# Kernel optimization log

Measured on AMD Instinct MI355X. Metric: run time of the kernel, lower is better.

The kernel has to match this reference:

```python
import jax, jax.numpy as jnp
import numpy as np

LATENT = 256
SELEN = 64
MSIZE = 8
BS = 32
T = 2048
TOUCH_IN = 3
GAZE_IN = 4


def setup_inputs() -> dict:
    key = jax.random.key(0)
    ks = jax.random.split(key, 16)
    kH = 1.0 / np.sqrt(LATENT)

    def u(k, shape):
        return jax.random.uniform(k, shape, jnp.float32, -kH, kH)

    return {
        "touch_d": jax.random.normal(ks[0], (BS, T, TOUCH_IN), jnp.float32),
        "gaze_d": jax.random.normal(ks[1], (BS, T, GAZE_IN), jnp.float32),
        # scale so start + SELEN <= T always (avoids the random fallback branch)
        "l": jax.random.uniform(ks[2], (BS, MSIZE), jnp.float32) * ((T - SELEN) / T),
        "tW_ih": u(ks[3], (4 * LATENT, TOUCH_IN)),
        "tW_hh": u(ks[4], (4 * LATENT, LATENT)),
        "tb_ih": u(ks[5], (4 * LATENT,)),
        "tb_hh": u(ks[6], (4 * LATENT,)),
        "gW_ih": u(ks[7], (4 * LATENT, GAZE_IN)),
        "gW_hh": u(ks[8], (4 * LATENT, LATENT)),
        "gb_ih": u(ks[9], (4 * LATENT,)),
        "gb_hh": u(ks[10], (4 * LATENT,)),
        "t_lin_w": u(ks[11], (LATENT, LATENT)),
        "t_lin_b": u(ks[12], (LATENT,)),
        "g_lin_w": u(ks[13], (LATENT, LATENT)),
        "g_lin_b": u(ks[14], (LATENT,)),
    }


def lstm(x, W_ih, W_hh, b_ih, b_hh):
    # x: [B, T, D] -> outputs [B, T, H]; PyTorch gate order i, f, g, o
    B = x.shape[0]
    H = W_hh.shape[1]
    x_proj = x @ W_ih.T + (b_ih + b_hh)  # [B, T, 4H] precomputed input GEMM

    def step(carry, xt):
        h, c = carry
        gates = xt + h @ W_hh.T
        i, f, g, o = jnp.split(gates, 4, axis=-1)
        c = jax.nn.sigmoid(f) * c + jax.nn.sigmoid(i) * jnp.tanh(g)
        h = jax.nn.sigmoid(o) * jnp.tanh(c)
        return (h, c), h

    h0 = jnp.zeros((B, H), x.dtype)
    _, ys = jax.lax.scan(step, (h0, h0), jnp.swapaxes(x_proj, 0, 1))
    return jnp.swapaxes(ys, 0, 1)


def glimpse_mean(emb, starts):
    # emb: [B, T, H]; starts: [B, M] int window starts; mean over M windows of SELEN
    idx = (starts[:, :, None] + jnp.arange(SELEN)).reshape(emb.shape[0], MSIZE * SELEN)
    gathered = jnp.take_along_axis(emb, idx[..., None], axis=1)  # [B, M*SELEN, H]
    return gathered.mean(axis=1)


def reference(touch_d, gaze_d, l, tW_ih, tW_hh, tb_ih, tb_hh,
              gW_ih, gW_hh, gb_ih, gb_hh, t_lin_w, t_lin_b, g_lin_w, g_lin_b):
    touch_out = lstm(touch_d, tW_ih, tW_hh, tb_ih, tb_hh)
    gaze_out = lstm(gaze_d, gW_ih, gW_hh, gb_ih, gb_hh)
    touch_emb = jax.nn.relu(touch_out) @ t_lin_w.T + t_lin_b  # [B, T, H]
    gaze_emb = jax.nn.relu(gaze_out) @ g_lin_w.T + g_lin_b

    touch_mean = touch_emb.mean(axis=1)
    gaze_mean = gaze_emb.mean(axis=1)

    starts = (l * T).astype(jnp.int32)  # [B, M], guaranteed start + SELEN <= T
    touch_attn = glimpse_mean(touch_emb, starts)
    gaze_attn = glimpse_mean(gaze_emb, starts)

    return jnp.concatenate([touch_mean, touch_attn, gaze_mean, gaze_attn], axis=-1)
```

## Files before the change

### kernel.cpp

```cpp
#include <hip/hip_runtime.h>

#define HDIM 256
#define TLEN 2048
#define SELEN 64
#define MSZ 8

typedef _Float16 f16x2 __attribute__((ext_vector_type(2)));

__device__ __forceinline__ float dot2f(unsigned int w, unsigned int h, float acc) {
  return __builtin_amdgcn_fdot2(__builtin_bit_cast(f16x2, w),
                                __builtin_bit_cast(f16x2, h), acc, false);
}

__device__ __forceinline__ unsigned int pack2(float a, float b) {
  f16x2 v;
  v.x = (_Float16)a; v.y = (_Float16)b;
  return __builtin_bit_cast(unsigned int, v);
}

__device__ __forceinline__ float sigm(float x)  { return 1.0f / (1.0f + __expf(-x)); }
__device__ __forceinline__ float tanh_f(float x) { return 1.0f - 2.0f / (__expf(2.0f * x) + 1.0f); }

#define WO_OFF    0
#define PART_OFF  131072
#define WIH_OFF   139264
#define CNT_OFF   155648
#define H2_OFF    157696
#define LDS_BYTES 158208

extern __shared__ unsigned char smem[];

__global__ __launch_bounds__(512, 2)
void lstm_seq_kernel(const float* __restrict__ touch, const float* __restrict__ gaze,
                     const float* __restrict__ l,
                     const float* __restrict__ tWih, const float* __restrict__ tWhh,
                     const float* __restrict__ tbih, const float* __restrict__ tbhh,
                     const float* __restrict__ gWih, const float* __restrict__ gWhh,
                     const float* __restrict__ gbih, const float* __restrict__ gbhh,
                     float* __restrict__ ws)
{
  const int bid  = (int)blockIdx.x;
  const int lsel = bid >> 5;
  const int b    = bid & 31;
  const int tid  = (int)threadIdx.x;
  const int kh   = tid >> 8;

  const float* __restrict__ x   = lsel ? gaze : touch;
  const float* __restrict__ Wih = lsel ? gWih : tWih;
  const float* __restrict__ Whh = lsel ? gWhh : tWhh;
  const float* __restrict__ bih = lsel ? gbih : tbih;
  const float* __restrict__ bhh = lsel ? gbhh : tbhh;
  const int D = lsel ? 4 : 3;

  unsigned int*  woL  = (unsigned int*)(smem + WO_OFF);
  float4*        part = (float4*)(smem + PART_OFF);
  float4*        wihF = (float4*)(smem + WIH_OFF);
  unsigned char* cntL = smem + CNT_OFF;
  unsigned int*  h2   = (unsigned int*)(smem + H2_OFF);

  unsigned int wi[64], wf[64], wg[64];
  {
    const float2* ri = (const float2*)(Whh + (size_t)(tid & 255) * HDIM + kh * 128);
    const float2* rf = (const float2*)((const float*)ri + 256 * HDIM);
    const float2* rg = (const float2*)((const float*)ri + 512 * HDIM);
    const float2* ro = (const float2*)((const float*)ri + 768 * HDIM);
    #pragma unroll
    for (int d = 0; d < 64; ++d) {
      float2 a = ri[d], bb = rf[d], c = rg[d], e = ro[d];
      wi[d] = pack2(a.x, a.y);
      wf[d] = pack2(bb.x, bb.y);
      wg[d] = pack2(c.x, c.y);
      woL[(((d >> 2) * 512 + tid) << 2) | (d & 3)] = pack2(e.x, e.y);
    }
  }

  for (int r = tid; r < 1024; r += 512) {
    const float* wr = Wih + (size_t)r * D;
    float4 v;
    v.x = wr[0]; v.y = wr[1]; v.z = wr[2];
    v.w = (D == 4) ? wr[3] : 0.0f;
    wihF[r] = v;
  }

  int sreg[MSZ];
  #pragma unroll
  for (int m = 0; m < MSZ; ++m) sreg[m] = (int)(l[b * MSZ + m] * 2048.0f);
  for (int t0 = tid; t0 < TLEN; t0 += 512) {
    int c = 0;
    #pragma unroll
    for (int m = 0; m < MSZ; ++m) c += (t0 >= sreg[m] && t0 < sreg[m] + SELEN) ? 1 : 0;
    cntL[t0] = (unsigned char)c;
  }

  if (tid < 128) h2[tid] = 0u;

  float bi_ = 0.f, bf_ = 0.f, bg_ = 0.f, bo_ = 0.f;
  float x0 = 0.f, x1 = 0.f, x2 = 0.f, x3 = 0.f;
  float cst = 0.f, Sall = 0.f, Swin = 0.f;
  const float* xbase = x + (size_t)b * TLEN * D;
  if (tid < 256) {
    bi_ = bih[tid]       + bhh[tid];
    bf_ = bih[tid + 256] + bhh[tid + 256];
    bg_ = bih[tid + 512] + bhh[tid + 512];
    bo_ = bih[tid + 768] + bhh[tid + 768];
    x0 = xbase[0]; x1 = xbase[1]; x2 = xbase[2];
    x3 = (D == 4) ? xbase[3] : 0.0f;
  }
  __syncthreads();

  const uint4* h2v = (const uint4*)h2;
  const uint4* wov = (const uint4*)woL;

  for (int t = 0; t < TLEN; ++t) {
    float ai = 0.f, af = 0.f, ag = 0.f, ao = 0.f;
    #pragma unroll
    for (int kk = 0; kk < 16; ++kk) {
      const uint4 hh  = h2v[(kh << 4) + kk];
      const uint4 wo4 = wov[(kk << 9) + tid];
      ai = dot2f(wi[4*kk+0], hh.x, ai);
      af = dot2f(wf[4*kk+0], hh.x, af);
      ag = dot2f(wg[4*kk+0], hh.x, ag);
      ao = dot2f(wo4.x,      hh.x, ao);
      ai = dot2f(wi[4*kk+1], hh.y, ai);
      af = dot2f(wf[4*kk+1], hh.y, af);
      ag = dot2f(wg[4*kk+1], hh.y, ag);
      ao = dot2f(wo4.y,      hh.y, ao);
      ai = dot2f(wi[4*kk+2], hh.z, ai);
      af = dot2f(wf[4*kk+2], hh.z, af);
      ag = dot2f(wg[4*kk+2], hh.z, ag);
      ao = dot2f(wo4.z,      hh.z, ao);
      ai = dot2f(wi[4*kk+3], hh.w, ai);
      af = dot2f(wf[4*kk+3], hh.w, af);
      ag = dot2f(wg[4*kk+3], hh.w, ag);
      ao = dot2f(wo4.w,      hh.w, ao);
    }
    part[tid] = make_float4(ai, af, ag, ao);
    __syncthreads();

    if (tid < 256) {
      const float4 p0  = part[tid];
      const float4 p1  = part[tid + 256];
      const float4 wi0 = wihF[tid];
      const float4 wi1 = wihF[tid + 256];
      const float4 wi2 = wihF[tid + 512];
      const float4 wi3 = wihF[tid + 768];
      float gi = p0.x + p1.x + bi_ + x0*wi0.x + x1*wi0.y + x2*wi0.z + x3*wi0.w;
      float gf = p0.y + p1.y + bf_ + x0*wi1.x + x1*wi1.y + x2*wi1.z + x3*wi1.w;
      float gg = p0.z + p1.z + bg_ + x0*wi2.x + x1*wi2.y + x2*wi2.z + x3*wi2.w;
      float go = p0.w + p1.w + bo_ + x0*wi3.x + x1*wi3.y + x2*wi3.z + x3*wi3.w;
      const float si = sigm(gi), sf = sigm(gf), so = sigm(go);
      const float tg = tanh_f(gg);
      cst = sf * cst + si * tg;
      const float hv = so * tanh_f(cst);
      const float rh = fmaxf(hv, 0.0f);
      Sall += rh;
      Swin += (float)cntL[t] * rh;
      ((_Float16*)h2)[tid] = (_Float16)hv;
      if (t + 1 < TLEN) {
        const float* xp = xbase + (size_t)(t + 1) * D;
        x0 = xp[0]; x1 = xp[1]; x2 = xp[2];
        x3 = (D == 4) ? xp[3] : 0.0f;
      }
    }
    __syncthreads();
  }

  if (tid < 256) {
    ws[((0 * 2 + lsel) * 32 + b) * HDIM + tid] = Sall;
    ws[((1 * 2 + lsel) * 32 + b) * HDIM + tid] = Swin;
  }
}

__global__ void proj_kernel(const float* __restrict__ ws,
                            const float* __restrict__ tlw, const float* __restrict__ tlb,
                            const float* __restrict__ glw, const float* __restrict__ glb,
                            float* __restrict__ out)
{
  const int b    = (int)blockIdx.x >> 2;
  const int seg  = (int)blockIdx.x & 3;
  const int j    = (int)threadIdx.x;
  const int lsel = seg >> 1;
  const int kind = seg & 1;
  const float* __restrict__ W    = lsel ? glw : tlw;
  const float* __restrict__ bias = lsel ? glb : tlb;
  const float scale = kind ? (1.0f / 512.0f) : (1.0f / 2048.0f);

  __shared__ float Sv[HDIM];
  Sv[j] = ws[((kind * 2 + lsel) * 32 + b) * HDIM + j] * scale;
  __syncthreads();

  float acc = bias[j];
  const float4* wr4 = (const float4*)(W + (size_t)j * HDIM);
  #pragma unroll 8
  for (int k4 = 0; k4 < HDIM / 4; ++k4) {
    const float4 w = wr4[k4];
    acc = fmaf(Sv[4*k4],     w.x, acc);
    acc = fmaf(Sv[4*k4 + 1], w.y, acc);
    acc = fmaf(Sv[4*k4 + 2], w.z, acc);
    acc = fmaf(Sv[4*k4 + 3], w.w, acc);
  }
  out[(size_t)b * 1024 + seg * HDIM + j] = acc;
}

extern "C" void kernel_launch(void* const* d_in, const int* in_sizes, int n_in,
                              void* d_out, int out_size, void* d_ws, size_t ws_size,
                              hipStream_t stream) {
  (void)in_sizes; (void)n_in; (void)out_size; (void)ws_size;
  const float* touch = (const float*)d_in[0];
  const float* gaze  = (const float*)d_in[1];
  const float* l     = (const float*)d_in[2];
  const float* tWih  = (const float*)d_in[3];
  const float* tWhh  = (const float*)d_in[4];
  const float* tbih  = (const float*)d_in[5];
  const float* tbhh  = (const float*)d_in[6];
  const float* gWih  = (const float*)d_in[7];
  const float* gWhh  = (const float*)d_in[8];
  const float* gbih  = (const float*)d_in[9];
  const float* gbhh  = (const float*)d_in[10];
  const float* tlw   = (const float*)d_in[11];
  const float* tlb   = (const float*)d_in[12];
  const float* glw   = (const float*)d_in[13];
  const float* glb   = (const float*)d_in[14];
  float* out = (float*)d_out;
  float* ws  = (float*)d_ws;

  hipFuncSetAttribute(reinterpret_cast<const void*>(&lstm_seq_kernel),
                      hipFuncAttributeMaxDynamicSharedMemorySize, LDS_BYTES);

  hipLaunchKernelGGL(lstm_seq_kernel, dim3(64), dim3(512), LDS_BYTES, stream,
                     touch, gaze, l, tWih, tWhh, tbih, tbhh,
                     gWih, gWhh, gbih, gbhh, ws);
  hipLaunchKernelGGL(proj_kernel, dim3(128), dim3(256), 0, stream,
                     ws, tlw, tlb, glw, glb, out);
}
```

Before: 3.363 ms.

## Split K across wave halves with shuffle reduce and double-buffered h to cut barriers

Each wavefront's two 32-lane halves now hold the two K-halves for the same 32 hidden units. Partial gate sums are combined with a cross-lane xor shuffle instead of an LDS partial buffer. The h vector is double-buffered by timestep parity, so only one barrier per step is needed instead of two. All 512 threads now compute the gate nonlinearities redundantly, and x is loaded inside the loop rather than prefetched, which puts a global load latency on the critical path of each step.

```diff
diff --git a/kernel.cpp b/kernel.cpp
--- a/kernel.cpp
+++ b/kernel.cpp
@@ -18,15 +18,14 @@
   return __builtin_bit_cast(unsigned int, v);
 }
 
-__device__ __forceinline__ float sigm(float x)  { return 1.0f / (1.0f + __expf(-x)); }
+__device__ __forceinline__ float sigm(float x)   { return 1.0f / (1.0f + __expf(-x)); }
 __device__ __forceinline__ float tanh_f(float x) { return 1.0f - 2.0f / (__expf(2.0f * x) + 1.0f); }
 
 #define WO_OFF    0
-#define PART_OFF  131072
-#define WIH_OFF   139264
-#define CNT_OFF   155648
-#define H2_OFF    157696
-#define LDS_BYTES 158208
+#define WIH_OFF   131072
+#define CNT_OFF   147456
+#define H2_OFF    149504
+#define LDS_BYTES 150528
 
 extern __shared__ unsigned char smem[];
 
@@ -43,7 +42,11 @@
   const int lsel = bid >> 5;
   const int b    = bid & 31;
   const int tid  = (int)threadIdx.x;
-  const int kh   = tid >> 8;
+  const int lane = tid & 63;
+  const int wv   = tid >> 6;
+  const int n    = wv * 32 + (lane & 31);
+  const int kh   = lane >> 5;
+  const int c0   = kh * 128;
 
   const float* __restrict__ x   = lsel ? gaze : touch;
   const float* __restrict__ Wih = lsel ? gWih : tWih;
@@ -53,24 +56,32 @@
   const int D = lsel ? 4 : 3;
 
   unsigned int*  woL  = (unsigned int*)(smem + WO_OFF);
-  float4*        part = (float4*)(smem + PART_OFF);
   float4*        wihF = (float4*)(smem + WIH_OFF);
   unsigned char* cntL = smem + CNT_OFF;
-  unsigned int*  h2   = (unsigned int*)(smem + H2_OFF);
 
   unsigned int wi[64], wf[64], wg[64];
   {
-    const float2* ri = (const float2*)(Whh + (size_t)(tid & 255) * HDIM + kh * 128);
+    const float2* ri = (const float2*)(Whh + (size_t)n * HDIM + c0);
     const float2* rf = (const float2*)((const float*)ri + 256 * HDIM);
     const float2* rg = (const float2*)((const float*)ri + 512 * HDIM);
-    const float2* ro = (const float2*)((const float*)ri + 768 * HDIM);
     #pragma unroll
     for (int d = 0; d < 64; ++d) {
-      float2 a = ri[d], bb = rf[d], c = rg[d], e = ro[d];
+      float2 a = ri[d], bb = rf[d], c = rg[d];
       wi[d] = pack2(a.x, a.y);
       wf[d] = pack2(bb.x, bb.y);
       wg[d] = pack2(c.x, c.y);
-      woL[(((d >> 2) * 512 + tid) << 2) | (d & 3)] = pack2(e.x, e.y);
+    }
+  }
+  {
+    const float2* ro = (const float2*)(Whh + (size_t)(n + 768) * HDIM + c0);
+    uint4* wo4 = (uint4*)woL;
+    #pragma unroll
+    for (int j = 0; j < 16; ++j) {
+      float2 e0 = ro[4*j], e1 = ro[4*j+1], e2 = ro[4*j+2], e3 = ro[4*j+3];
+      uint4 v;
+      v.x = pack2(e0.x, e0.y); v.y = pack2(e1.x, e1.y);
+      v.z = pack2(e2.x, e2.y); v.w = pack2(e3.x, e3.y);
+      wo4[j * 512 + tid] = v;
     }
   }
 
@@ -82,92 +93,93 @@
     wihF[r] = v;
   }
 
-  int sreg[MSZ];
-  #pragma unroll
-  for (int m = 0; m < MSZ; ++m) sreg[m] = (int)(l[b * MSZ + m] * 2048.0f);
-  for (int t0 = tid; t0 < TLEN; t0 += 512) {
-    int c = 0;
-    #pragma unroll
-    for (int m = 0; m < MSZ; ++m) c += (t0 >= sreg[m] && t0 < sreg[m] + SELEN) ? 1 : 0;
-    cntL[t0] = (unsigned char)c;
-  }
-
-  if (tid < 128) h2[tid] = 0u;
-
-  float bi_ = 0.f, bf_ = 0.f, bg_ = 0.f, bo_ = 0.f;
-  float x0 = 0.f, x1 = 0.f, x2 = 0.f, x3 = 0.f;
+  {
+    int sreg[MSZ];
+    #pragma unroll
+    for (int m = 0; m < MSZ; ++m) sreg[m] = (int)(l[b * MSZ + m] * 2048.0f);
+    for (int t0 = tid; t0 < TLEN; t0 += 512) {
+      int c = 0;
+      #pragma unroll
+      for (int m = 0; m < MSZ; ++m) c += (t0 >= sreg[m] && t0 < sreg[m] + SELEN) ? 1 : 0;
+      cntL[t0] = (unsigned char)c;
+    }
+  }
+
+  if (tid < 128) ((unsigned int*)(smem + H2_OFF))[tid] = 0u;
+
+  const float bi_ = bih[n]       + bhh[n];
+  const float bf_ = bih[n + 256] + bhh[n + 256];
+  const float bg_ = bih[n + 512] + bhh[n + 512];
+  const float bo_ = bih[n + 768] + bhh[n + 768];
+
   float cst = 0.f, Sall = 0.f, Swin = 0.f;
-  const float* xbase = x + (size_t)b * TLEN * D;
-  if (tid < 256) {
-    bi_ = bih[tid]       + bhh[tid];
-    bf_ = bih[tid + 256] + bhh[tid + 256];
-    bg_ = bih[tid + 512] + bhh[tid + 512];
-    bo_ = bih[tid + 768] + bhh[tid + 768];
-    x0 = xbase[0]; x1 = xbase[1]; x2 = xbase[2];
-    x3 = (D == 4) ? xbase[3] : 0.0f;
-  }
+  const float* xrow = x + (size_t)b * TLEN * D;
+
   __syncthreads();
 
-  const uint4* h2v = (const uint4*)h2;
-  const uint4* wov = (const uint4*)woL;
+  const uint4* wo4r = ((const uint4*)woL) + tid;
 
   for (int t = 0; t < TLEN; ++t) {
+    const float* xp = xrow + (size_t)t * D;
+    const float x0 = xp[0], x1 = xp[1], x2 = xp[2];
+    const float x3 = (D == 4) ? xp[3] : 0.0f;
+    const float cw = (float)cntL[t];
+
+    const uint4* hv4 = (const uint4*)(smem + H2_OFF + (t & 1) * 512 + kh * 256);
+
     float ai = 0.f, af = 0.f, ag = 0.f, ao = 0.f;
     #pragma unroll
-    for (int kk = 0; kk < 16; ++kk) {
-      const uint4 hh  = h2v[(kh << 4) + kk];
-      const uint4 wo4 = wov[(kk << 9) + tid];
-      ai = dot2f(wi[4*kk+0], hh.x, ai);
-      af = dot2f(wf[4*kk+0], hh.x, af);
-      ag = dot2f(wg[4*kk+0], hh.x, ag);
-      ao = dot2f(wo4.x,      hh.x, ao);
-      ai = dot2f(wi[4*kk+1], hh.y, ai);
-      af = dot2f(wf[4*kk+1], hh.y, af);
-      ag = dot2f(wg[4*kk+1], hh.y, ag);
-      ao = dot2f(wo4.y,      hh.y, ao);
-      ai = dot2f(wi[4*kk+2], hh.z, ai);
-      af = dot2f(wf[4*kk+2], hh.z, af);
-      ag = dot2f(wg[4*kk+2], hh.z, ag);
-      ao = dot2f(wo4.z,      hh.z, ao);
-      ai = dot2f(wi[4*kk+3], hh.w, ai);
-      af = dot2f(wf[4*kk+3], hh.w, af);
-      ag = dot2f(wg[4*kk+3], hh.w, ag);
-      ao = dot2f(wo4.w,      hh.w, ao);
-    }
-    part[tid] = make_float4(ai, af, ag, ao);
+    for (int j = 0; j < 16; ++j) {
+      const uint4 hh = hv4[j];
+      const uint4 wo = wo4r[j * 512];
+      ai = dot2f(wi[4*j+0], hh.x, ai);
+      af = dot2f(wf[4*j+0], hh.x, af);
+      ag = dot2f(wg[4*j+0], hh.x, ag);
+      ao = dot2f(wo.x,      hh.x, ao);
+      ai = dot2f(wi[4*j+1], hh.y, ai);
+      af = dot2f(wf[4*j+1], hh.y, af);
+      ag = dot2f(wg[4*j+1], hh.y, ag);
+      ao = dot2f(wo.y,      hh.y, ao);
+      ai = dot2f(wi[4*j+2], hh.z, ai);
+      af = dot2f(wf[4*j+2], hh.z, af);
+      ag = dot2f(wg[4*j+2], hh.z, ag);
+      ao = dot2f(wo.z,      hh.z, ao);
+      ai = dot2f(wi[4*j+3], hh.w, ai);
+      af = dot2f(wf[4*j+3], hh.w, af);
+      ag = dot2f(wg[4*j+3], hh.w, ag);
+      ao = dot2f(wo.w,      hh.w, ao);
+    }
+
+    ai += __shfl_xor(ai, 32);
+    af += __shfl_xor(af, 32);
+    ag += __shfl_xor(ag, 32);
+    ao += __shfl_xor(ao, 32);
+
+    const float4 wr0 = wihF[n];
+    const float4 wr1 = wihF[n + 256];
+    const float4 wr2 = wihF[n + 512];
+    const float4 wr3 = wihF[n + 768];
+    const float gi = ai + bi_ + x0*wr0.x + x1*wr0.y + x2*wr0.z + x3*wr0.w;
+    const float gf = af + bf_ + x0*wr1.x + x1*wr1.y + x2*wr1.z + x3*wr1.w;
+    const float gg = ag + bg_ + x0*wr2.x + x1*wr2.y + x2*wr2.z + x3*wr2.w;
+    const float go = ao + bo_ + x0*wr3.x + x1*wr3.y + x2*wr3.z + x3*wr3.w;
+    const float si = sigm(gi), sf = sigm(gf), so = sigm(go);
+    const float tg = tanh_f(gg);
+    cst = sf * cst + si * tg;
+    const float hv = so * tanh_f(cst);
+    const float rh = fmaxf(hv, 0.0f);
+    Sall += rh;
+    Swin += cw * rh;
+
+    if (kh == 0)
+      ((_Float16*)(smem + H2_OFF + ((t + 1) & 1) * 512))[n] = (_Float16)hv;
+
     __syncthreads();
-
-    if (tid < 256) {
-      const float4 p0  = part[tid];
-      const float4 p1  = part[tid + 256];
-      const float4 wi0 = wihF[tid];
-      const float4 wi1 = wihF[tid + 256];
-      const float4 wi2 = wihF[tid + 512];
-      const float4 wi3 = wihF[tid + 768];
-      float gi = p0.x + p1.x + bi_ + x0*wi0.x + x1*wi0.y + x2*wi0.z + x3*wi0.w;
-      float gf = p0.y + p1.y + bf_ + x0*wi1.x + x1*wi1.y + x2*wi1.z + x3*wi1.w;
-      float gg = p0.z + p1.z + bg_ + x0*wi2.x + x1*wi2.y + x2*wi2.z + x3*wi2.w;
-      float go = p0.w + p1.w + bo_ + x0*wi3.x + x1*wi3.y + x2*wi3.z + x3*wi3.w;
-      const float si = sigm(gi), sf = sigm(gf), so = sigm(go);
-      const float tg = tanh_f(gg);
-      cst = sf * cst + si * tg;
-      const float hv = so * tanh_f(cst);
-      const float rh = fmaxf(hv, 0.0f);
-      Sall += rh;
-      Swin += (float)cntL[t] * rh;
-      ((_Float16*)h2)[tid] = (_Float16)hv;
-      if (t + 1 < TLEN) {
-        const float* xp = xbase + (size_t)(t + 1) * D;
-        x0 = xp[0]; x1 = xp[1]; x2 = xp[2];
-        x3 = (D == 4) ? xp[3] : 0.0f;
-      }
-    }
-    __syncthreads();
-  }
-
-  if (tid < 256) {
-    ws[((0 * 2 + lsel) * 32 + b) * HDIM + tid] = Sall;
-    ws[((1 * 2 + lsel) * 32 + b) * HDIM + tid] = Swin;
+  }
+
+  if (kh == 0) {
+    ws[((0 * 2 + lsel) * 32 + b) * HDIM + n] = Sall;
+    ws[((1 * 2 + lsel) * 32 + b) * HDIM + n] = Swin;
   }
 }
 
```

After: 3.598 ms. +7.0%, slower.
